# Performance work log

Measured on AMD Instinct MI355X. Metric: run time of the kernel, lower is better.

## Reference

```python
import jax, jax.numpy as jnp
import numpy as np

INPUT_SIZE = 1024
HIDDEN_SIZE = 1024
BATCH = 8192
MLP_H1, MLP_H2 = 16, 8


def _uniform(key, shape, stdv):
    return jax.random.uniform(key, shape, jnp.float32, -stdv, stdv)


def setup_inputs() -> dict:
    key = jax.random.key(0)
    ks = jax.random.split(key, 20)
    stdv = 1.0 / np.sqrt(HIDDEN_SIZE)
    I, H = INPUT_SIZE, HIDDEN_SIZE
    inp = {
        "x": jax.random.normal(ks[0], (BATCH, I), jnp.float32),
        "h": jax.random.normal(ks[1], (BATCH, H), jnp.float32),
        "c": jax.random.normal(ks[2], (BATCH, H), jnp.float32),
        # gate weights (torch layout: matmul(h, W_h*) + matmul(x, W_x*) + b)
        "W_hi": _uniform(ks[3], (H, H), stdv),
        "W_xi": _uniform(ks[4], (I, H), stdv),
        "b_i": _uniform(ks[5], (H,), stdv),
        "W_hc": _uniform(ks[6], (H, H), stdv),
        "W_xc": _uniform(ks[7], (I, H), stdv),
        "b_c": _uniform(ks[8], (H,), stdv),
        "W_ho": _uniform(ks[9], (H, H), stdv),
        "W_xo": _uniform(ks[10], (I, H), stdv),
        "b_o": _uniform(ks[11], (H,), stdv),
        # forget MLP: (I+H) -> 16 -> 8 -> H, ReLU hidden, sigmoid output
        "W1": _uniform(ks[12], (I + H, MLP_H1), stdv),
        "b1": _uniform(ks[13], (MLP_H1,), stdv),
        "W2": _uniform(ks[14], (MLP_H1, MLP_H2), stdv),
        "b2": _uniform(ks[15], (MLP_H2,), stdv),
        "W3": _uniform(ks[16], (MLP_H2, H), stdv),
        "b3": _uniform(ks[17], (H,), stdv),
    }
    return inp


def reference(x, h, c, W_hi, W_xi, b_i, W_hc, W_xc, b_c, W_ho, W_xo, b_o,
              W1, b1, W2, b2, W3, b3):
    # forget gate via small MLP on concat(x, h)
    xh = jnp.concatenate((x, h), axis=1)           # [B, I+H]
    z = jax.nn.relu(xh @ W1 + b1)                  # [B, 16]
    z = jax.nn.relu(z @ W2 + b2)                   # [B, 8]
    f = jax.nn.sigmoid(z @ W3 + b3)                # [B, H]

    i = jax.nn.sigmoid(h @ W_hi + x @ W_xi + b_i)
    g = jnp.tanh(h @ W_hc + x @ W_xc + b_c)
    o = jax.nn.sigmoid(h @ W_ho + x @ W_xo + b_o)

    c_new = f * c + i * g
    h_new = o * jnp.tanh(c_new)
    return (h_new, c_new, f)
```

## Files before the change

kernel.cpp:

```cpp
#include <hip/hip_runtime.h>
#include <math.h>

#define BATCH 8192
#define HDIM  1024
#define KDIM  2048
#define NDIM  3072

typedef __attribute__((ext_vector_type(8))) short short8;
typedef __attribute__((ext_vector_type(4))) float floatx4;

__device__ __forceinline__ float b2f(unsigned short u) {
  union { unsigned int i; float f; } v; v.i = ((unsigned int)u) << 16; return v.f;
}
__device__ __forceinline__ unsigned short f2b(float f) {
  union { unsigned int i; float f; } v; v.f = f;
  unsigned int r = v.i + 0x7FFFu + ((v.i >> 16) & 1u);
  return (unsigned short)(r >> 16);
}
__device__ __forceinline__ float ldsel(const void* p, size_t i, int isbf) {
  return isbf ? b2f(((const unsigned short*)p)[i]) : ((const float*)p)[i];
}
__device__ __forceinline__ float sigf(float x) { return 1.0f / (1.0f + __expf(-x)); }
__device__ __forceinline__ float tanhfast(float x) {
  float a = __builtin_fabsf(x);
  float t = __expf(-2.f * a);
  float r = (1.f - t) / (1.f + t);
  return copysignf(r, x);
}

__device__ __forceinline__ void gld16(const void* g, void* l) {
  auto gp = reinterpret_cast<__attribute__((address_space(1))) unsigned int*>(
      (unsigned long long)g);
  auto lp = reinterpret_cast<__attribute__((address_space(3))) unsigned int*>(
      (unsigned long long)l);
  __builtin_amdgcn_global_load_lds(gp, lp, 16, 0, 0);
}

__global__ void k_detect(const unsigned int* __restrict__ x, int* __restrict__ flag) {
  unsigned int w = x[threadIdx.x];
  unsigned short lo = (unsigned short)(w & 0xFFFFu);
  int e = (lo >> 7) & 0xFF;
  bool ok = (e >= 110 && e <= 135) || ((lo & 0x7FFFu) == 0);
  unsigned long long m = __ballot(ok);
  if (threadIdx.x == 0) *flag = (__popcll(m) >= 48) ? 1 : 0;
}

__global__ __launch_bounds__(256) void k_pack_w(
    const void* __restrict__ wxi, const void* __restrict__ whi,
    const void* __restrict__ wxc, const void* __restrict__ whc,
    const void* __restrict__ wxo, const void* __restrict__ who,
    unsigned short* __restrict__ WT, const int* __restrict__ flag) {
  const int isbf = *flag;
  const int bx = blockIdx.x;
  const int mat = bx >> 8;
  const int rem = bx & 255;
  const int ti = rem >> 4;
  const int tj = rem & 15;
  const void* Ws[6] = {wxi, whi, wxc, whc, wxo, who};
  const void* W = Ws[mat];
  const int gt = mat >> 1;
  const int half = mat & 1;
  __shared__ float tbuf[64][65];
  const int t = threadIdx.x;
  const int rrow = t >> 3;
  const int c8 = (t & 7) * 8;
#pragma unroll
  for (int it = 0; it < 2; ++it) {
    int row = it * 32 + rrow;
    size_t off = (size_t)(ti * 64 + row) * 1024 + tj * 64 + c8;
    if (isbf) {
      const unsigned short* s = (const unsigned short*)W + off;
      ushort4 a = *(const ushort4*)(s);
      ushort4 b = *(const ushort4*)(s + 4);
      tbuf[row][c8+0]=b2f(a.x); tbuf[row][c8+1]=b2f(a.y);
      tbuf[row][c8+2]=b2f(a.z); tbuf[row][c8+3]=b2f(a.w);
      tbuf[row][c8+4]=b2f(b.x); tbuf[row][c8+5]=b2f(b.y);
      tbuf[row][c8+6]=b2f(b.z); tbuf[row][c8+7]=b2f(b.w);
    } else {
      const float* s = (const float*)W + off;
      float4 a = *(const float4*)(s);
      float4 b = *(const float4*)(s + 4);
      tbuf[row][c8+0]=a.x; tbuf[row][c8+1]=a.y; tbuf[row][c8+2]=a.z; tbuf[row][c8+3]=a.w;
      tbuf[row][c8+4]=b.x; tbuf[row][c8+5]=b.y; tbuf[row][c8+6]=b.z; tbuf[row][c8+7]=b.w;
    }
  }
  __syncthreads();
#pragma unroll
  for (int it = 0; it < 2; ++it) {
    int nl = it * 32 + rrow;
    int n = gt * 1024 + tj * 64 + nl;
    int kb = half * 1024 + ti * 64 + c8;
    short8 pk;
#pragma unroll
    for (int i = 0; i < 8; ++i) pk[i] = (short)f2b(tbuf[c8 + i][nl]);
    *(short8*)(WT + (size_t)n * KDIM + kb) = pk;
  }
}

__global__ __launch_bounds__(256) void k_pack_small(
    const void* __restrict__ W1, unsigned short* __restrict__ W1T,
    const int* __restrict__ flag) {
  const int isbf = *flag;
  const int t = threadIdx.x;
  for (int k = t; k < 2048; k += 256) {
    unsigned short v[16];
    if (isbf) {
      const unsigned short* r = (const unsigned short*)W1 + (size_t)k * 16;
#pragma unroll
      for (int i = 0; i < 16; ++i) v[i] = r[i];
    } else {
      const float* r = (const float*)W1 + (size_t)k * 16;
#pragma unroll
      for (int i = 0; i < 16; ++i) v[i] = f2b(r[i]);
    }
#pragma unroll
    for (int nn = 0; nn < 16; ++nn) W1T[(size_t)nn * 2048 + k] = v[nn];
  }
}

__global__ __launch_bounds__(256) void k_pack_a(
    const void* __restrict__ x, const void* __restrict__ h,
    unsigned short* __restrict__ A, const int* __restrict__ flag) {
  if (*flag) return;
  size_t idx = ((size_t)blockIdx.x * 256 + threadIdx.x) * 8;
  int k = (int)(idx & 2047);
  size_t m = idx >> 11;
  const float* s = (k < 1024) ? (const float*)x + m * 1024 + k
                              : (const float*)h + m * 1024 + (k - 1024);
  float4 a = *(const float4*)(s);
  float4 b = *(const float4*)(s + 4);
  short8 pk;
  pk[0]=(short)f2b(a.x); pk[1]=(short)f2b(a.y); pk[2]=(short)f2b(a.z); pk[3]=(short)f2b(a.w);
  pk[4]=(short)f2b(b.x); pk[5]=(short)f2b(b.y); pk[6]=(short)f2b(b.z); pk[7]=(short)f2b(b.w);
  *(short8*)(A + idx) = pk;
}

__global__ __launch_bounds__(256, 3) void k_gemm(
    const void* __restrict__ x, const void* __restrict__ h,
    const unsigned short* __restrict__ Apack,
    const unsigned short* __restrict__ WT,
    unsigned short* __restrict__ P, const int* __restrict__ flag) {
  const int isbf = *flag;
  const unsigned short* Ax = isbf ? (const unsigned short*)x : Apack;
  const unsigned short* Ah = isbf ? (const unsigned short*)h : (Apack + 1024);
  const int sA = isbf ? 1024 : 2048;
  __shared__ __align__(16) unsigned short lA[128 * 64];
  __shared__ __align__(16) unsigned short lB[128 * 64];
  const int tid = threadIdx.x;
  const int lane = tid & 63;
  const int wv = tid >> 6;
  const int wm = (wv >> 1) << 6;
  const int wn = (wv & 1) << 6;
  const int m0 = blockIdx.y << 7;
  const int n0 = blockIdx.x << 7;

  floatx4 acc[4][4];
  const floatx4 fzero = {0.f, 0.f, 0.f, 0.f};
#pragma unroll
  for (int i = 0; i < 4; ++i)
#pragma unroll
    for (int j = 0; j < 4; ++j) acc[i][j] = fzero;

  int rr[4], kk[4];
#pragma unroll
  for (int ps = 0; ps < 4; ++ps) {
    int chunk = ps * 256 + tid;
    rr[ps] = chunk >> 3;
    kk[ps] = (chunk & 7) ^ (rr[ps] & 7);
  }
  const int px0 = (lane >> 4) ^ (lane & 7);
  const int px1 = ((lane >> 4) + 4) ^ (lane & 7);
  const int rowA = wm + (lane & 15);
  const int rowB = wn + (lane & 15);

  for (int kt = 0; kt < KDIM / 64; ++kt) {
    const int k0 = kt * 64;
    const unsigned short* Abase = (k0 < 1024) ? (Ax + k0) : (Ah + (k0 - 1024));
#pragma unroll
    for (int ps = 0; ps < 4; ++ps) {
      const int chunk = ps * 256 + tid;
      gld16(Abase + (size_t)(m0 + rr[ps]) * sA + kk[ps] * 8, lA + chunk * 8);
      gld16(WT + ((size_t)(n0 + rr[ps]) * KDIM + k0 + kk[ps] * 8), lB + chunk * 8);
    }
    __syncthreads();
#pragma unroll
    for (int s = 0; s < 2; ++s) {
      const int px = s ? px1 : px0;
      short8 af[4], bfr[4];
#pragma unroll
      for (int i = 0; i < 4; ++i)
        af[i] = *(const short8*)(lA + ((((rowA + (i << 4)) << 3) + px) << 3));
#pragma unroll
      for (int i = 0; i < 4; ++i)
        bfr[i] = *(const short8*)(lB + ((((rowB + (i << 4)) << 3) + px) << 3));
#pragma unroll
      for (int mi = 0; mi < 4; ++mi)
#pragma unroll
        for (int ni = 0; ni < 4; ++ni)
          acc[mi][ni] = __builtin_amdgcn_mfma_f32_16x16x32_bf16(
              af[mi], bfr[ni], acc[mi][ni], 0, 0, 0);
    }
    __syncthreads();
  }
  const int col = lane & 15;
  const int rq = (lane >> 4) << 2;
#pragma unroll
  for (int mi = 0; mi < 4; ++mi) {
#pragma unroll
    for (int ni = 0; ni < 4; ++ni) {
      const size_t n = (size_t)(n0 + wn + (ni << 4) + col);
#pragma unroll
      for (int t = 0; t < 4; ++t) {
        const size_t m = (size_t)(m0 + wm + (mi << 4) + rq + t);
        P[m * NDIM + n] = f2b(acc[mi][ni][t]);
      }
    }
  }
}

__global__ __launch_bounds__(64) void k_z2(
    const void* __restrict__ x, const void* __restrict__ h,
    const unsigned short* __restrict__ Apack,
    const unsigned short* __restrict__ W1T,
    const void* __restrict__ b1, const void* __restrict__ W2,
    const void* __restrict__ b2, float* __restrict__ z2,
    const int* __restrict__ flag) {
  const int isbf = *flag;
  const unsigned short* Ax = isbf ? (const unsigned short*)x : Apack;
  const unsigned short* Ah = isbf ? (const unsigned short*)h : (Apack + 1024);
  const int sA = isbf ? 1024 : 2048;
  const int lane = threadIdx.x;
  const int m0 = blockIdx.x * 16;
  const int q = lane >> 4;
  const int r = lane & 15;
  floatx4 acc = {0.f, 0.f, 0.f, 0.f};
  const unsigned short* arow0 = Ax + (size_t)(m0 + r) * sA;
  const unsigned short* arow1 = Ah + (size_t)(m0 + r) * sA;
  const unsigned short* brow = W1T + (size_t)r * 2048;
#pragma unroll 4
  for (int kt = 0; kt < 32; ++kt) {
    int k = kt * 32 + q * 8;
    short8 a = *(const short8*)(arow0 + k);
    short8 b = *(const short8*)(brow + k);
    acc = __builtin_amdgcn_mfma_f32_16x16x32_bf16(a, b, acc, 0, 0, 0);
  }
#pragma unroll 4
  for (int kt = 0; kt < 32; ++kt) {
    int k = kt * 32 + q * 8;
    short8 a = *(const short8*)(arow1 + k);
    short8 b = *(const short8*)(brow + 1024 + k);
    acc = __builtin_amdgcn_mfma_f32_16x16x32_bf16(a, b, acc, 0, 0, 0);
  }
  __shared__ float z1s[16][17];
  float b1f = ldsel(b1, (size_t)r, isbf);
#pragma unroll
  for (int t = 0; t < 4; ++t) z1s[q * 4 + t][r] = fmaxf(acc[t] + b1f, 0.f);
  __syncthreads();
  const int row = lane >> 2;
  const int p2 = (lane & 3) * 2;
  float s0 = ldsel(b2, (size_t)p2, isbf);
  float s1 = ldsel(b2, (size_t)p2 + 1, isbf);
#pragma unroll
  for (int nn = 0; nn < 16; ++nn) {
    float z = z1s[row][nn];
    s0 += z * ldsel(W2, (size_t)nn * 8 + p2, isbf);
    s1 += z * ldsel(W2, (size_t)nn * 8 + p2 + 1, isbf);
  }
  float2 o = make_float2(fmaxf(s0, 0.f), fmaxf(s1, 0.f));
  *(float2*)(z2 + (size_t)(m0 + row) * 8 + p2) = o;
}

__global__ __launch_bounds__(256) void k_pointwise(
    const unsigned short* __restrict__ P, const void* __restrict__ cin,
    const void* __restrict__ bi, const void* __restrict__ bc,
    const void* __restrict__ bo, const float* __restrict__ z2,
    const void* __restrict__ W3, const void* __restrict__ b3,
    void* __restrict__ out, const int* __restrict__ flag) {
  const int isbf = *flag;
  const size_t MH = (size_t)BATCH * HDIM;
  const size_t m = blockIdx.x;
  const int n = threadIdx.x * 4;
  const size_t idx = m * 1024 + n;
  const unsigned short* pr = P + m * NDIM + n;
  ushort4 ui = *(const ushort4*)(pr);
  ushort4 ug = *(const ushort4*)(pr + 1024);
  ushort4 uo = *(const ushort4*)(pr + 2048);
  float pi[4] = {b2f(ui.x), b2f(ui.y), b2f(ui.z), b2f(ui.w)};
  float pg[4] = {b2f(ug.x), b2f(ug.y), b2f(ug.z), b2f(ug.w)};
  float po[4] = {b2f(uo.x), b2f(uo.y), b2f(uo.z), b2f(uo.w)};
  float4 za = *(const float4*)(z2 + m * 8);
  float4 zb = *(const float4*)(z2 + m * 8 + 4);
  float zz[8] = {za.x, za.y, za.z, za.w, zb.x, zb.y, zb.z, zb.w};
  float f3[4];
  float bif[4], bcf[4], bof[4], cf[4];
  if (isbf) {
    ushort4 u3 = *(const ushort4*)((const unsigned short*)b3 + n);
    f3[0]=b2f(u3.x); f3[1]=b2f(u3.y); f3[2]=b2f(u3.z); f3[3]=b2f(u3.w);
#pragma unroll
    for (int j = 0; j < 8; ++j) {
      ushort4 w = *(const ushort4*)((const unsigned short*)W3 + (size_t)j * 1024 + n);
      f3[0] += zz[j]*b2f(w.x); f3[1] += zz[j]*b2f(w.y);
      f3[2] += zz[j]*b2f(w.z); f3[3] += zz[j]*b2f(w.w);
    }
    ushort4 a = *(const ushort4*)((const unsigned short*)bi + n);
    ushort4 b = *(const ushort4*)((const unsigned short*)bc + n);
    ushort4 d = *(const ushort4*)((const unsigned short*)bo + n);
    ushort4 e = *(const ushort4*)((const unsigned short*)cin + idx);
    bif[0]=b2f(a.x); bif[1]=b2f(a.y); bif[2]=b2f(a.z); bif[3]=b2f(a.w);
    bcf[0]=b2f(b.x); bcf[1]=b2f(b.y); bcf[2]=b2f(b.z); bcf[3]=b2f(b.w);
    bof[0]=b2f(d.x); bof[1]=b2f(d.y); bof[2]=b2f(d.z); bof[3]=b2f(d.w);
    cf[0]=b2f(e.x);  cf[1]=b2f(e.y);  cf[2]=b2f(e.z);  cf[3]=b2f(e.w);
  } else {
    float4 u3 = *(const float4*)((const float*)b3 + n);
    f3[0]=u3.x; f3[1]=u3.y; f3[2]=u3.z; f3[3]=u3.w;
#pragma unroll
    for (int j = 0; j < 8; ++j) {
      float4 w = *(const float4*)((const float*)W3 + (size_t)j * 1024 + n);
      f3[0] += zz[j]*w.x; f3[1] += zz[j]*w.y; f3[2] += zz[j]*w.z; f3[3] += zz[j]*w.w;
    }
    float4 a = *(const float4*)((const float*)bi + n);
    float4 b = *(const float4*)((const float*)bc + n);
    float4 d = *(const float4*)((const float*)bo + n);
    float4 e = *(const float4*)((const float*)cin + idx);
    bif[0]=a.x; bif[1]=a.y; bif[2]=a.z; bif[3]=a.w;
    bcf[0]=b.x; bcf[1]=b.y; bcf[2]=b.z; bcf[3]=b.w;
    bof[0]=d.x; bof[1]=d.y; bof[2]=d.z; bof[3]=d.w;
    cf[0]=e.x;  cf[1]=e.y;  cf[2]=e.z;  cf[3]=e.w;
  }
  float hn[4], cn[4], ff[4];
#pragma unroll
  for (int t = 0; t < 4; ++t) {
    float F = sigf(f3[t]);
    float I = sigf(pi[t] + bif[t]);
    float G = tanhfast(pg[t] + bcf[t]);
    float O = sigf(po[t] + bof[t]);
    float C = F * cf[t] + I * G;
    ff[t] = F;
    cn[t] = C;
    hn[t] = O * tanhfast(C);
  }
  if (isbf) {
    unsigned short* ob = (unsigned short*)out;
    *(ushort4*)(ob + idx) = make_ushort4(f2b(hn[0]), f2b(hn[1]), f2b(hn[2]), f2b(hn[3]));
    *(ushort4*)(ob + MH + idx) = make_ushort4(f2b(cn[0]), f2b(cn[1]), f2b(cn[2]), f2b(cn[3]));
    *(ushort4*)(ob + 2 * MH + idx) = make_ushort4(f2b(ff[0]), f2b(ff[1]), f2b(ff[2]), f2b(ff[3]));
  } else {
    float* ob = (float*)out;
    *(float4*)(ob + idx) = make_float4(hn[0], hn[1], hn[2], hn[3]);
    *(float4*)(ob + MH + idx) = make_float4(cn[0], cn[1], cn[2], cn[3]);
    *(float4*)(ob + 2 * MH + idx) = make_float4(ff[0], ff[1], ff[2], ff[3]);
  }
}

extern "C" void kernel_launch(void* const* d_in, const int* in_sizes, int n_in,
                              void* d_out, int out_size, void* d_ws, size_t ws_size,
                              hipStream_t stream) {
  const void* x    = d_in[0];
  const void* h    = d_in[1];
  const void* c    = d_in[2];
  const void* W_hi = d_in[3];
  const void* W_xi = d_in[4];
  const void* b_i  = d_in[5];
  const void* W_hc = d_in[6];
  const void* W_xc = d_in[7];
  const void* b_c  = d_in[8];
  const void* W_ho = d_in[9];
  const void* W_xo = d_in[10];
  const void* b_o  = d_in[11];
  const void* W1   = d_in[12];
  const void* b1   = d_in[13];
  const void* W2   = d_in[14];
  const void* b2   = d_in[15];
  const void* W3   = d_in[16];
  const void* b3   = d_in[17];

  char* ws = (char*)d_ws;
  unsigned short* A   = (unsigned short*)ws;
  unsigned short* WT  = (unsigned short*)(ws + 33554432);
  unsigned short* P   = (unsigned short*)(ws + 46137344);
  float*          z2b = (float*)(ws + 96468992);
  unsigned short* W1T = (unsigned short*)(ws + 96731136);
  int*           flag = (int*)(ws + 96796672);

  k_detect<<<dim3(1), dim3(64), 0, stream>>>((const unsigned int*)x, flag);
  k_pack_w<<<dim3(6 * 256), dim3(256), 0, stream>>>(W_xi, W_hi, W_xc, W_hc,
                                                    W_xo, W_ho, WT, flag);
  k_pack_small<<<dim3(1), dim3(256), 0, stream>>>(W1, W1T, flag);
  k_pack_a<<<dim3(8192), dim3(256), 0, stream>>>(x, h, A, flag);
  k_gemm<<<dim3(NDIM / 128, BATCH / 128), dim3(256), 0, stream>>>(x, h, A, WT, P, flag);
  k_z2<<<dim3(BATCH / 16), dim3(64), 0, stream>>>(x, h, A, W1T, b1, W2, b2, z2b, flag);
  k_pointwise<<<dim3(BATCH), dim3(256), 0, stream>>>(P, c, b_i, b_c, b_o, z2b,
                                                     W3, b3, d_out, flag);
}
```

Baseline: 383.5 us.

## Fuse LSTM pointwise epilogue into gate GEMM and merge pack kernels

The GEMM now computes all three gates for a 128x64 hidden tile per block, loading 3x64 weight rows into LDS. It applies the LSTM cell pointwise math directly from registers, so the bf16 pre-activation buffer P and the separate pointwise kernel are removed. The detect, weight-pack, W1-pack and activation-pack kernels are merged into one launch, and dtype detection is recomputed per block instead of read from a flag. k_z2 now splits K across 4 waves and reduces through shared memory. The cost is scattered scalar epilogue stores and loads (c, out) with poor coalescing, plus more accumulator registers per thread.

```diff
diff --git a/kernel.cpp b/kernel.cpp
--- a/kernel.cpp
+++ b/kernel.cpp
@@ -4,7 +4,6 @@
 #define BATCH 8192
 #define HDIM  1024
 #define KDIM  2048
-#define NDIM  3072
 
 typedef __attribute__((ext_vector_type(8))) short short8;
 typedef __attribute__((ext_vector_type(4))) float floatx4;
@@ -19,6 +18,10 @@
 }
 __device__ __forceinline__ float ldsel(const void* p, size_t i, int isbf) {
   return isbf ? b2f(((const unsigned short*)p)[i]) : ((const float*)p)[i];
+}
+__device__ __forceinline__ void stsel(void* p, size_t i, int isbf, float v) {
+  if (isbf) ((unsigned short*)p)[i] = f2b(v);
+  else ((float*)p)[i] = v;
 }
 __device__ __forceinline__ float sigf(float x) { return 1.0f / (1.0f + __expf(-x)); }
 __device__ __forceinline__ float tanhfast(float x) {
@@ -28,6 +31,15 @@
   return copysignf(r, x);
 }
 
+__device__ __forceinline__ int detect_bf(const void* x) {
+  unsigned int w = ((const unsigned int*)x)[threadIdx.x & 63];
+  unsigned short lo = (unsigned short)(w & 0xFFFFu);
+  int e = (lo >> 7) & 0xFF;
+  bool ok = (e >= 110 && e <= 135) || ((lo & 0x7FFFu) == 0);
+  unsigned long long m = __ballot(ok);
+  return (__popcll(m) >= 48) ? 1 : 0;
+}
+
 __device__ __forceinline__ void gld16(const void* g, void* l) {
   auto gp = reinterpret_cast<__attribute__((address_space(1))) unsigned int*>(
       (unsigned long long)g);
@@ -36,138 +48,175 @@
   __builtin_amdgcn_global_load_lds(gp, lp, 16, 0, 0);
 }
 
-__global__ void k_detect(const unsigned int* __restrict__ x, int* __restrict__ flag) {
-  unsigned int w = x[threadIdx.x];
-  unsigned short lo = (unsigned short)(w & 0xFFFFu);
-  int e = (lo >> 7) & 0xFF;
-  bool ok = (e >= 110 && e <= 135) || ((lo & 0x7FFFu) == 0);
-  unsigned long long m = __ballot(ok);
-  if (threadIdx.x == 0) *flag = (__popcll(m) >= 48) ? 1 : 0;
-}
-
-__global__ __launch_bounds__(256) void k_pack_w(
+__global__ __launch_bounds__(256) void k_pack(
+    const void* __restrict__ x, const void* __restrict__ h,
     const void* __restrict__ wxi, const void* __restrict__ whi,
     const void* __restrict__ wxc, const void* __restrict__ whc,
     const void* __restrict__ wxo, const void* __restrict__ who,
-    unsigned short* __restrict__ WT, const int* __restrict__ flag) {
-  const int isbf = *flag;
+    const void* __restrict__ W1,
+    unsigned short* __restrict__ WT, unsigned short* __restrict__ W1T,
+    unsigned short* __restrict__ A) {
+  const int isbf = detect_bf(x);
   const int bx = blockIdx.x;
-  const int mat = bx >> 8;
-  const int rem = bx & 255;
-  const int ti = rem >> 4;
-  const int tj = rem & 15;
-  const void* Ws[6] = {wxi, whi, wxc, whc, wxo, who};
-  const void* W = Ws[mat];
-  const int gt = mat >> 1;
-  const int half = mat & 1;
-  __shared__ float tbuf[64][65];
   const int t = threadIdx.x;
-  const int rrow = t >> 3;
-  const int c8 = (t & 7) * 8;
-#pragma unroll
-  for (int it = 0; it < 2; ++it) {
-    int row = it * 32 + rrow;
-    size_t off = (size_t)(ti * 64 + row) * 1024 + tj * 64 + c8;
-    if (isbf) {
-      const unsigned short* s = (const unsigned short*)W + off;
-      ushort4 a = *(const ushort4*)(s);
-      ushort4 b = *(const ushort4*)(s + 4);
-      tbuf[row][c8+0]=b2f(a.x); tbuf[row][c8+1]=b2f(a.y);
-      tbuf[row][c8+2]=b2f(a.z); tbuf[row][c8+3]=b2f(a.w);
-      tbuf[row][c8+4]=b2f(b.x); tbuf[row][c8+5]=b2f(b.y);
-      tbuf[row][c8+6]=b2f(b.z); tbuf[row][c8+7]=b2f(b.w);
-    } else {
-      const float* s = (const float*)W + off;
-      float4 a = *(const float4*)(s);
-      float4 b = *(const float4*)(s + 4);
-      tbuf[row][c8+0]=a.x; tbuf[row][c8+1]=a.y; tbuf[row][c8+2]=a.z; tbuf[row][c8+3]=a.w;
-      tbuf[row][c8+4]=b.x; tbuf[row][c8+5]=b.y; tbuf[row][c8+6]=b.z; tbuf[row][c8+7]=b.w;
-    }
-  }
+  if (bx < 1536) {
+    const int mat = bx >> 8;
+    const int rem = bx & 255;
+    const int ti = rem >> 4;
+    const int tj = rem & 15;
+    const void* Ws[6] = {wxi, whi, wxc, whc, wxo, who};
+    const void* W = Ws[mat];
+    const int gt = mat >> 1;
+    const int half = mat & 1;
+    __shared__ float tbuf[64][65];
+    const int rrow = t >> 3;
+    const int c8 = (t & 7) * 8;
+#pragma unroll
+    for (int it = 0; it < 2; ++it) {
+      int row = it * 32 + rrow;
+      size_t off = (size_t)(ti * 64 + row) * 1024 + tj * 64 + c8;
+      if (isbf) {
+        const unsigned short* s = (const unsigned short*)W + off;
+        ushort4 a = *(const ushort4*)(s);
+        ushort4 b = *(const ushort4*)(s + 4);
+        tbuf[row][c8+0]=b2f(a.x); tbuf[row][c8+1]=b2f(a.y);
+        tbuf[row][c8+2]=b2f(a.z); tbuf[row][c8+3]=b2f(a.w);
+        tbuf[row][c8+4]=b2f(b.x); tbuf[row][c8+5]=b2f(b.y);
+        tbuf[row][c8+6]=b2f(b.z); tbuf[row][c8+7]=b2f(b.w);
+      } else {
+        const float* s = (const float*)W + off;
+        float4 a = *(const float4*)(s);
+        float4 b = *(const float4*)(s + 4);
+        tbuf[row][c8+0]=a.x; tbuf[row][c8+1]=a.y; tbuf[row][c8+2]=a.z; tbuf[row][c8+3]=a.w;
+        tbuf[row][c8+4]=b.x; tbuf[row][c8+5]=b.y; tbuf[row][c8+6]=b.z; tbuf[row][c8+7]=b.w;
+      }
+    }
+    __syncthreads();
+#pragma unroll
+    for (int it = 0; it < 2; ++it) {
+      int nl = it * 32 + rrow;
+      int n = gt * 1024 + tj * 64 + nl;
+      int kb = half * 1024 + ti * 64 + c8;
+      short8 pk;
+#pragma unroll
+      for (int i = 0; i < 8; ++i) pk[i] = (short)f2b(tbuf[c8 + i][nl]);
+      *(short8*)(WT + (size_t)n * KDIM + kb) = pk;
+    }
+  } else if (bx == 1536) {
+    for (int k = t; k < 2048; k += 256) {
+      unsigned short v[16];
+      if (isbf) {
+        const unsigned short* r = (const unsigned short*)W1 + (size_t)k * 16;
+#pragma unroll
+        for (int i = 0; i < 16; ++i) v[i] = r[i];
+      } else {
+        const float* r = (const float*)W1 + (size_t)k * 16;
+#pragma unroll
+        for (int i = 0; i < 16; ++i) v[i] = f2b(r[i]);
+      }
+#pragma unroll
+      for (int nn = 0; nn < 16; ++nn) W1T[(size_t)nn * 2048 + k] = v[nn];
+    }
+  } else {
+    if (isbf) return;
+    size_t idx = ((size_t)(bx - 1537) * 256 + t) * 8;
+    int k = (int)(idx & 2047);
+    size_t m = idx >> 11;
+    const float* s = (k < 1024) ? (const float*)x + m * 1024 + k
+                                : (const float*)h + m * 1024 + (k - 1024);
+    float4 a = *(const float4*)(s);
+    float4 b = *(const float4*)(s + 4);
+    short8 pk;
+    pk[0]=(short)f2b(a.x); pk[1]=(short)f2b(a.y); pk[2]=(short)f2b(a.z); pk[3]=(short)f2b(a.w);
+    pk[4]=(short)f2b(b.x); pk[5]=(short)f2b(b.y); pk[6]=(short)f2b(b.z); pk[7]=(short)f2b(b.w);
+    *(short8*)(A + idx) = pk;
+  }
+}
+
+__global__ __launch_bounds__(256) void k_z2(
+    const void* __restrict__ x, const void* __restrict__ h,
+    const unsigned short* __restrict__ Apack,
+    const unsigned short* __restrict__ W1T,
+    const void* __restrict__ b1, const void* __restrict__ W2,
+    const void* __restrict__ b2, float* __restrict__ z2) {
+  const int isbf = detect_bf(x);
+  const unsigned short* Ax = isbf ? (const unsigned short*)x : Apack;
+  const unsigned short* Ah = isbf ? (const unsigned short*)h : (Apack + 1024);
+  const int sA = isbf ? 1024 : 2048;
+  const int tid = threadIdx.x;
+  const int w = tid >> 6;
+  const int lane = tid & 63;
+  const int q = lane >> 4;
+  const int r = lane & 15;
+  const int m0 = blockIdx.x * 16;
+  const unsigned short* ar =
+      ((w >> 1) ? Ah : Ax) + (size_t)(m0 + r) * sA + (w & 1) * 512;
+  const unsigned short* br = W1T + (size_t)r * 2048 + (w >> 1) * 1024 + (w & 1) * 512;
+  floatx4 acc = {0.f, 0.f, 0.f, 0.f};
+#pragma unroll 4
+  for (int kt = 0; kt < 16; ++kt) {
+    int k = kt * 32 + q * 8;
+    short8 a = *(const short8*)(ar + k);
+    short8 b = *(const short8*)(br + k);
+    acc = __builtin_amdgcn_mfma_f32_16x16x32_bf16(a, b, acc, 0, 0, 0);
+  }
+  __shared__ float part[4][16][17];
+  __shared__ float z1s[16][17];
+#pragma unroll
+  for (int t = 0; t < 4; ++t) part[w][q * 4 + t][r] = acc[t];
   __syncthreads();
-#pragma unroll
-  for (int it = 0; it < 2; ++it) {
-    int nl = it * 32 + rrow;
-    int n = gt * 1024 + tj * 64 + nl;
-    int kb = half * 1024 + ti * 64 + c8;
-    short8 pk;
-#pragma unroll
-    for (int i = 0; i < 8; ++i) pk[i] = (short)f2b(tbuf[c8 + i][nl]);
-    *(short8*)(WT + (size_t)n * KDIM + kb) = pk;
-  }
-}
-
-__global__ __launch_bounds__(256) void k_pack_small(
-    const void* __restrict__ W1, unsigned short* __restrict__ W1T,
-    const int* __restrict__ flag) {
-  const int isbf = *flag;
-  const int t = threadIdx.x;
-  for (int k = t; k < 2048; k += 256) {
-    unsigned short v[16];
-    if (isbf) {
-      const unsigned short* r = (const unsigned short*)W1 + (size_t)k * 16;
-#pragma unroll
-      for (int i = 0; i < 16; ++i) v[i] = r[i];
-    } else {
-      const float* r = (const float*)W1 + (size_t)k * 16;
-#pragma unroll
-      for (int i = 0; i < 16; ++i) v[i] = f2b(r[i]);
-    }
-#pragma unroll
-    for (int nn = 0; nn < 16; ++nn) W1T[(size_t)nn * 2048 + k] = v[nn];
-  }
-}
-
-__global__ __launch_bounds__(256) void k_pack_a(
-    const void* __restrict__ x, const void* __restrict__ h,
-    unsigned short* __restrict__ A, const int* __restrict__ flag) {
-  if (*flag) return;
-  size_t idx = ((size_t)blockIdx.x * 256 + threadIdx.x) * 8;
-  int k = (int)(idx & 2047);
-  size_t m = idx >> 11;
-  const float* s = (k < 1024) ? (const float*)x + m * 1024 + k
-                              : (const float*)h + m * 1024 + (k - 1024);
-  float4 a = *(const float4*)(s);
-  float4 b = *(const float4*)(s + 4);
-  short8 pk;
-  pk[0]=(short)f2b(a.x); pk[1]=(short)f2b(a.y); pk[2]=(short)f2b(a.z); pk[3]=(short)f2b(a.w);
-  pk[4]=(short)f2b(b.x); pk[5]=(short)f2b(b.y); pk[6]=(short)f2b(b.z); pk[7]=(short)f2b(b.w);
-  *(short8*)(A + idx) = pk;
-}
-
-__global__ __launch_bounds__(256, 3) void k_gemm(
+  {
+    const int row = tid >> 4;
+    const int n = tid & 15;
+    float s = part[0][row][n] + part[1][row][n] + part[2][row][n] +
+              part[3][row][n] + ldsel(b1, (size_t)n, isbf);
+    z1s[row][n] = fmaxf(s, 0.f);
+  }
+  __syncthreads();
+  if (tid < 128) {
+    const int row = tid >> 3;
+    const int p = tid & 7;
+    float s = ldsel(b2, (size_t)p, isbf);
+#pragma unroll
+    for (int nn = 0; nn < 16; ++nn)
+      s += z1s[row][nn] * ldsel(W2, (size_t)nn * 8 + p, isbf);
+    z2[(size_t)(m0 + row) * 8 + p] = fmaxf(s, 0.f);
+  }
+}
+
+__global__ __launch_bounds__(256, 3) void k_gemm_fused(
     const void* __restrict__ x, const void* __restrict__ h,
     const unsigned short* __restrict__ Apack,
     const unsigned short* __restrict__ WT,
-    unsigned short* __restrict__ P, const int* __restrict__ flag) {
-  const int isbf = *flag;
+    const void* __restrict__ cin,
+    const void* __restrict__ bi, const void* __restrict__ bc,
+    const void* __restrict__ bo,
+    const float* __restrict__ z2,
+    const void* __restrict__ W3, const void* __restrict__ b3,
+    void* __restrict__ out) {
+  const int isbf = detect_bf(x);
   const unsigned short* Ax = isbf ? (const unsigned short*)x : Apack;
   const unsigned short* Ah = isbf ? (const unsigned short*)h : (Apack + 1024);
   const int sA = isbf ? 1024 : 2048;
   __shared__ __align__(16) unsigned short lA[128 * 64];
-  __shared__ __align__(16) unsigned short lB[128 * 64];
+  __shared__ __align__(16) unsigned short lB[3 * 64 * 64];
   const int tid = threadIdx.x;
   const int lane = tid & 63;
   const int wv = tid >> 6;
   const int wm = (wv >> 1) << 6;
-  const int wn = (wv & 1) << 6;
-  const int m0 = blockIdx.y << 7;
-  const int n0 = blockIdx.x << 7;
-
-  floatx4 acc[4][4];
+  const int wn = (wv & 1) << 5;
+  const int m0 = (blockIdx.x & 63) << 7;
+  const int n0h = (blockIdx.x >> 6) << 6;
+
+  floatx4 acc[3][4][2];
   const floatx4 fzero = {0.f, 0.f, 0.f, 0.f};
 #pragma unroll
-  for (int i = 0; i < 4; ++i)
-#pragma unroll
-    for (int j = 0; j < 4; ++j) acc[i][j] = fzero;
-
-  int rr[4], kk[4];
-#pragma unroll
-  for (int ps = 0; ps < 4; ++ps) {
-    int chunk = ps * 256 + tid;
-    rr[ps] = chunk >> 3;
-    kk[ps] = (chunk & 7) ^ (rr[ps] & 7);
-  }
+  for (int g = 0; g < 3; ++g)
+#pragma unroll
+    for (int i = 0; i < 4; ++i)
+#pragma unroll
+      for (int j = 0; j < 2; ++j) acc[g][i][j] = fzero;
+
   const int px0 = (lane >> 4) ^ (lane & 7);
   const int px1 = ((lane >> 4) + 4) ^ (lane & 7);
   const int rowA = wm + (lane & 15);
@@ -179,176 +228,77 @@
 #pragma unroll
     for (int ps = 0; ps < 4; ++ps) {
       const int chunk = ps * 256 + tid;
-      gld16(Abase + (size_t)(m0 + rr[ps]) * sA + kk[ps] * 8, lA + chunk * 8);
-      gld16(WT + ((size_t)(n0 + rr[ps]) * KDIM + k0 + kk[ps] * 8), lB + chunk * 8);
+      const int row = chunk >> 3;
+      const int kc = (chunk & 7) ^ (row & 7);
+      gld16(Abase + (size_t)(m0 + row) * sA + kc * 8, lA + chunk * 8);
+    }
+#pragma unroll
+    for (int ps = 0; ps < 6; ++ps) {
+      const int chunk = ps * 256 + tid;
+      const int g = chunk >> 9;
+      const int row = (chunk >> 3) & 63;
+      const int kc = (chunk & 7) ^ (row & 7);
+      gld16(WT + ((size_t)(g * 1024 + n0h + row) * KDIM + k0 + kc * 8),
+            lB + chunk * 8);
     }
     __syncthreads();
 #pragma unroll
     for (int s = 0; s < 2; ++s) {
       const int px = s ? px1 : px0;
-      short8 af[4], bfr[4];
+      short8 af[4];
 #pragma unroll
       for (int i = 0; i < 4; ++i)
         af[i] = *(const short8*)(lA + ((((rowA + (i << 4)) << 3) + px) << 3));
 #pragma unroll
-      for (int i = 0; i < 4; ++i)
-        bfr[i] = *(const short8*)(lB + ((((rowB + (i << 4)) << 3) + px) << 3));
-#pragma unroll
-      for (int mi = 0; mi < 4; ++mi)
-#pragma unroll
-        for (int ni = 0; ni < 4; ++ni)
-          acc[mi][ni] = __builtin_amdgcn_mfma_f32_16x16x32_bf16(
-              af[mi], bfr[ni], acc[mi][ni], 0, 0, 0);
+      for (int g = 0; g < 3; ++g) {
+        short8 b0 = *(const short8*)(lB + ((((g * 64 + rowB) << 3) + px) << 3));
+        short8 b1 = *(const short8*)(lB + ((((g * 64 + rowB + 16) << 3) + px) << 3));
+#pragma unroll
+        for (int mi = 0; mi < 4; ++mi) {
+          acc[g][mi][0] = __builtin_amdgcn_mfma_f32_16x16x32_bf16(
+              af[mi], b0, acc[g][mi][0], 0, 0, 0);
+          acc[g][mi][1] = __builtin_amdgcn_mfma_f32_16x16x32_bf16(
+              af[mi], b1, acc[g][mi][1], 0, 0, 0);
+        }
+      }
     }
     __syncthreads();
   }
+
+  const size_t MH = (size_t)BATCH * HDIM;
   const int col = lane & 15;
-  const int rq = (lane >> 4) << 2;
+  const int rbase = (lane >> 4) << 2;
 #pragma unroll
   for (int mi = 0; mi < 4; ++mi) {
 #pragma unroll
-    for (int ni = 0; ni < 4; ++ni) {
-      const size_t n = (size_t)(n0 + wn + (ni << 4) + col);
+    for (int ni = 0; ni < 2; ++ni) {
+      const int n = n0h + wn + (ni << 4) + col;
+      float w3v[8];
+#pragma unroll
+      for (int j = 0; j < 8; ++j) w3v[j] = ldsel(W3, (size_t)j * 1024 + n, isbf);
+      const float b3v = ldsel(b3, (size_t)n, isbf);
+      const float biv = ldsel(bi, (size_t)n, isbf);
+      const float bcv = ldsel(bc, (size_t)n, isbf);
+      const float bov = ldsel(bo, (size_t)n, isbf);
 #pragma unroll
       for (int t = 0; t < 4; ++t) {
-        const size_t m = (size_t)(m0 + wm + (mi << 4) + rq + t);
-        P[m * NDIM + n] = f2b(acc[mi][ni][t]);
+        const size_t m = (size_t)(m0 + wm + (mi << 4) + rbase + t);
+        const float* zr = z2 + m * 8;
+        float f3 = b3v;
+#pragma unroll
+        for (int j = 0; j < 8; ++j) f3 += zr[j] * w3v[j];
+        const float F = sigf(f3);
+        const float I = sigf(acc[0][mi][ni][t] + biv);
+        const float G = tanhfast(acc[1][mi][ni][t] + bcv);
+        const float O = sigf(acc[2][mi][ni][t] + bov);
+        const float cv = ldsel(cin, m * 1024 + n, isbf);
+        const float C = F * cv + I * G;
+        const float H = O * tanhfast(C);
+        stsel(out, m * 1024 + n, isbf, H);
+        stsel(out, MH + m * 1024 + n, isbf, C);
+        stsel(out, 2 * MH + m * 1024 + n, isbf, F);
       }
     }
-  }
-}
-
-__global__ __launch_bounds__(64) void k_z2(
-    const void* __restrict__ x, const void* __restrict__ h,
-    const unsigned short* __restrict__ Apack,
-    const unsigned short* __restrict__ W1T,
-    const void* __restrict__ b1, const void* __restrict__ W2,
-    const void* __restrict__ b2, float* __restrict__ z2,
-    const int* __restrict__ flag) {
-  const int isbf = *flag;
-  const unsigned short* Ax = isbf ? (const unsigned short*)x : Apack;
-  const unsigned short* Ah = isbf ? (const unsigned short*)h : (Apack + 1024);
-  const int sA = isbf ? 1024 : 2048;
-  const int lane = threadIdx.x;
-  const int m0 = blockIdx.x * 16;
-  const int q = lane >> 4;
-  const int r = lane & 15;
-  floatx4 acc = {0.f, 0.f, 0.f, 0.f};
-  const unsigned short* arow0 = Ax + (size_t)(m0 + r) * sA;
-  const unsigned short* arow1 = Ah + (size_t)(m0 + r) * sA;
-  const unsigned short* brow = W1T + (size_t)r * 2048;
-#pragma unroll 4
-  for (int kt = 0; kt < 32; ++kt) {
-    int k = kt * 32 + q * 8;
-    short8 a = *(const short8*)(arow0 + k);
-    short8 b = *(const short8*)(brow + k);
-    acc = __builtin_amdgcn_mfma_f32_16x16x32_bf16(a, b, acc, 0, 0, 0);
-  }
-#pragma unroll 4
-  for (int kt = 0; kt < 32; ++kt) {
-    int k = kt * 32 + q * 8;
-    short8 a = *(const short8*)(arow1 + k);
-    short8 b = *(const short8*)(brow + 1024 + k);
-    acc = __builtin_amdgcn_mfma_f32_16x16x32_bf16(a, b, acc, 0, 0, 0);
-  }
-  __shared__ float z1s[16][17];
-  float b1f = ldsel(b1, (size_t)r, isbf);
-#pragma unroll
-  for (int t = 0; t < 4; ++t) z1s[q * 4 + t][r] = fmaxf(acc[t] + b1f, 0.f);
-  __syncthreads();
-  const int row = lane >> 2;
-  const int p2 = (lane & 3) * 2;
-  float s0 = ldsel(b2, (size_t)p2, isbf);
-  float s1 = ldsel(b2, (size_t)p2 + 1, isbf);
-#pragma unroll
-  for (int nn = 0; nn < 16; ++nn) {
-    float z = z1s[row][nn];
-    s0 += z * ldsel(W2, (size_t)nn * 8 + p2, isbf);
-    s1 += z * ldsel(W2, (size_t)nn * 8 + p2 + 1, isbf);
-  }
-  float2 o = make_float2(fmaxf(s0, 0.f), fmaxf(s1, 0.f));
-  *(float2*)(z2 + (size_t)(m0 + row) * 8 + p2) = o;
-}
-
-__global__ __launch_bounds__(256) void k_pointwise(
-    const unsigned short* __restrict__ P, const void* __restrict__ cin,
-    const void* __restrict__ bi, const void* __restrict__ bc,
-    const void* __restrict__ bo, const float* __restrict__ z2,
-    const void* __restrict__ W3, const void* __restrict__ b3,
-    void* __restrict__ out, const int* __restrict__ flag) {
-  const int isbf = *flag;
-  const size_t MH = (size_t)BATCH * HDIM;
-  const size_t m = blockIdx.x;
-  const int n = threadIdx.x * 4;
-  const size_t idx = m * 1024 + n;
-  const unsigned short* pr = P + m * NDIM + n;
-  ushort4 ui = *(const ushort4*)(pr);
-  ushort4 ug = *(const ushort4*)(pr + 1024);
-  ushort4 uo = *(const ushort4*)(pr + 2048);
-  float pi[4] = {b2f(ui.x), b2f(ui.y), b2f(ui.z), b2f(ui.w)};
-  float pg[4] = {b2f(ug.x), b2f(ug.y), b2f(ug.z), b2f(ug.w)};
-  float po[4] = {b2f(uo.x), b2f(uo.y), b2f(uo.z), b2f(uo.w)};
-  float4 za = *(const float4*)(z2 + m * 8);
-  float4 zb = *(const float4*)(z2 + m * 8 + 4);
-  float zz[8] = {za.x, za.y, za.z, za.w, zb.x, zb.y, zb.z, zb.w};
-  float f3[4];
-  float bif[4], bcf[4], bof[4], cf[4];
-  if (isbf) {
-    ushort4 u3 = *(const ushort4*)((const unsigned short*)b3 + n);
-    f3[0]=b2f(u3.x); f3[1]=b2f(u3.y); f3[2]=b2f(u3.z); f3[3]=b2f(u3.w);
-#pragma unroll
-    for (int j = 0; j < 8; ++j) {
-      ushort4 w = *(const ushort4*)((const unsigned short*)W3 + (size_t)j * 1024 + n);
-      f3[0] += zz[j]*b2f(w.x); f3[1] += zz[j]*b2f(w.y);
-      f3[2] += zz[j]*b2f(w.z); f3[3] += zz[j]*b2f(w.w);
-    }
-    ushort4 a = *(const ushort4*)((const unsigned short*)bi + n);
-    ushort4 b = *(const ushort4*)((const unsigned short*)bc + n);
-    ushort4 d = *(const ushort4*)((const unsigned short*)bo + n);
-    ushort4 e = *(const ushort4*)((const unsigned short*)cin + idx);
-    bif[0]=b2f(a.x); bif[1]=b2f(a.y); bif[2]=b2f(a.z); bif[3]=b2f(a.w);
-    bcf[0]=b2f(b.x); bcf[1]=b2f(b.y); bcf[2]=b2f(b.z); bcf[3]=b2f(b.w);
-    bof[0]=b2f(d.x); bof[1]=b2f(d.y); bof[2]=b2f(d.z); bof[3]=b2f(d.w);
-    cf[0]=b2f(e.x);  cf[1]=b2f(e.y);  cf[2]=b2f(e.z);  cf[3]=b2f(e.w);
-  } else {
-    float4 u3 = *(const float4*)((const float*)b3 + n);
-    f3[0]=u3.x; f3[1]=u3.y; f3[2]=u3.z; f3[3]=u3.w;
-#pragma unroll
-    for (int j = 0; j < 8; ++j) {
-      float4 w = *(const float4*)((const float*)W3 + (size_t)j * 1024 + n);
-      f3[0] += zz[j]*w.x; f3[1] += zz[j]*w.y; f3[2] += zz[j]*w.z; f3[3] += zz[j]*w.w;
-    }
-    float4 a = *(const float4*)((const float*)bi + n);
-    float4 b = *(const float4*)((const float*)bc + n);
-    float4 d = *(const float4*)((const float*)bo + n);
-    float4 e = *(const float4*)((const float*)cin + idx);
-    bif[0]=a.x; bif[1]=a.y; bif[2]=a.z; bif[3]=a.w;
-    bcf[0]=b.x; bcf[1]=b.y; bcf[2]=b.z; bcf[3]=b.w;
-    bof[0]=d.x; bof[1]=d.y; bof[2]=d.z; bof[3]=d.w;
-    cf[0]=e.x;  cf[1]=e.y;  cf[2]=e.z;  cf[3]=e.w;
-  }
-  float hn[4], cn[4], ff[4];
-#pragma unroll
-  for (int t = 0; t < 4; ++t) {
-    float F = sigf(f3[t]);
-    float I = sigf(pi[t] + bif[t]);
-    float G = tanhfast(pg[t] + bcf[t]);
-    float O = sigf(po[t] + bof[t]);
-    float C = F * cf[t] + I * G;
-    ff[t] = F;
-    cn[t] = C;
-    hn[t] = O * tanhfast(C);
-  }
-  if (isbf) {
-    unsigned short* ob = (unsigned short*)out;
-    *(ushort4*)(ob + idx) = make_ushort4(f2b(hn[0]), f2b(hn[1]), f2b(hn[2]), f2b(hn[3]));
-    *(ushort4*)(ob + MH + idx) = make_ushort4(f2b(cn[0]), f2b(cn[1]), f2b(cn[2]), f2b(cn[3]));
-    *(ushort4*)(ob + 2 * MH + idx) = make_ushort4(f2b(ff[0]), f2b(ff[1]), f2b(ff[2]), f2b(ff[3]));
-  } else {
-    float* ob = (float*)out;
-    *(float4*)(ob + idx) = make_float4(hn[0], hn[1], hn[2], hn[3]);
-    *(float4*)(ob + MH + idx) = make_float4(cn[0], cn[1], cn[2], cn[3]);
-    *(float4*)(ob + 2 * MH + idx) = make_float4(ff[0], ff[1], ff[2], ff[3]);
   }
 }
 
@@ -377,18 +327,12 @@
   char* ws = (char*)d_ws;
   unsigned short* A   = (unsigned short*)ws;
   unsigned short* WT  = (unsigned short*)(ws + 33554432);
-  unsigned short* P   = (unsigned short*)(ws + 46137344);
-  float*          z2b = (float*)(ws + 96468992);
-  unsigned short* W1T = (unsigned short*)(ws + 96731136);
-  int*           flag = (int*)(ws + 96796672);
-
-  k_detect<<<dim3(1), dim3(64), 0, stream>>>((const unsigned int*)x, flag);
-  k_pack_w<<<dim3(6 * 256), dim3(256), 0, stream>>>(W_xi, W_hi, W_xc, W_hc,
-                                                    W_xo, W_ho, WT, flag);
-  k_pack_small<<<dim3(1), dim3(256), 0, stream>>>(W1, W1T, flag);
-  k_pack_a<<<dim3(8192), dim3(256), 0, stream>>>(x, h, A, flag);
-  k_gemm<<<dim3(NDIM / 128, BATCH / 128), dim3(256), 0, stream>>>(x, h, A, WT, P, flag);
-  k_z2<<<dim3(BATCH / 16), dim3(64), 0, stream>>>(x, h, A, W1T, b1, W2, b2, z2b, flag);
-  k_pointwise<<<dim3(BATCH), dim3(256), 0, stream>>>(P, c, b_i, b_c, b_o, z2b,
-                                                     W3, b3, d_out, flag);
-}
+  float*          z2b = (float*)(ws + 46137344);
+  unsigned short* W1T = (unsigned short*)(ws + 46399488);
+
+  k_pack<<<dim3(1537 + 8192), dim3(256), 0, stream>>>(
+      x, h, W_xi, W_hi, W_xc, W_hc, W_xo, W_ho, W1, WT, W1T, A);
+  k_z2<<<dim3(BATCH / 16), dim3(256), 0, stream>>>(x, h, A, W1T, b1, W2, b2, z2b);
+  k_gemm_fused<<<dim3(64 * 16), dim3(256), 0, stream>>>(
+      x, h, A, WT, c, b_i, b_c, b_o, z2b, W3, b3, d_out);
+}
```

Result: slower. 465.1 us (+21.3%).
